# Kernel tuning notes

Measured on AMD Instinct MI355X. Metric: run time of the kernel, lower is better.

## Reference

```python
import jax, jax.numpy as jnp
import numpy as np

EPS = 1e-6

def elu_feature_map(x):
    # phi(x) = elu(x) + 1 (always positive)
    return jax.nn.elu(x) + 1.0

def setup_inputs() -> dict:
    key = jax.random.key(0)
    kq, kk, kv = jax.random.split(key, 3)
    B, T, H, E = 2, 4096, 8, 64
    return {
        "query": jax.random.normal(kq, (B, T, H, E), dtype=jnp.float32),
        "key": jax.random.normal(kk, (B, T, H, E), dtype=jnp.float32),
        "value": jax.random.normal(kv, (B, T, H, E), dtype=jnp.float32),
    }

def reference(query, key, value):
    # b t h e -> b h t e
    q = jnp.transpose(query, (0, 2, 1, 3))
    k = jnp.transpose(key, (0, 2, 1, 3))
    v = jnp.transpose(value, (0, 2, 1, 3))
    Q = elu_feature_map(q)  # [b,h,t,e]
    K = elu_feature_map(k)  # [b,h,t,e]
    # Causal linear attention: running sums over the sequence axis.
    # KV_cum[t] = sum_{s<=t} K_s (outer) V_s  -> [b,h,t,e,d]
    kv = jnp.einsum('bhte,bhtd->bhted', K, v)
    kv_cum = jnp.cumsum(kv, axis=2)
    k_cum = jnp.cumsum(K, axis=2)  # [b,h,t,e]
    # Normalizer Z_t = 1 / (Q_t . sum_{s<=t} K_s + eps)
    Z = 1.0 / (jnp.einsum('bhte,bhte->bht', Q, k_cum) + EPS)
    out = jnp.einsum('bhte,bhted->bhtd', Q, kv_cum) * Z[..., None]
    # b h t d -> b t h d
    return jnp.transpose(out, (0, 2, 1, 3))
```

## Files before the change

kernel.cpp:

```cpp
#include <hip/hip_runtime.h>
#include <hip/hip_bf16.h>
#include <math.h>

#define B 2
#define T 4096
#define H 8
#define E 64
#define D 64
#define C 128
#define NC (T / C)
#define BH (B * H)
#define EPS 1e-6f
#define PT 132
#define PQ 72
#define PBT 200

typedef short short8 __attribute__((ext_vector_type(8)));
typedef float f32x4 __attribute__((ext_vector_type(4)));

__device__ __forceinline__ float phi(float x) {
    return x > 0.0f ? x + 1.0f : __expf(x);
}
__device__ __forceinline__ uint pk2(float a, float b) {
    __hip_bfloat162 h = __float22bfloat162_rn(make_float2(a, b));
    union { __hip_bfloat162 h2; uint u; } cv; cv.h2 = h; return cv.u;
}
__device__ __forceinline__ ushort f2bf(float f) {
    uint u = __float_as_uint(f);
    return (ushort)((u + 0x7FFFu + ((u >> 16) & 1u)) >> 16);
}
__device__ __forceinline__ float bf2f(ushort h) {
    return __uint_as_float(((uint)h) << 16);
}

__global__ __launch_bounds__(256) void k_chunk_sums(
        const float* __restrict__ Kg, const float* __restrict__ Vg,
        ushort* __restrict__ SpartBf, float* __restrict__ zpart,
        ushort* __restrict__ VTg, ushort* __restrict__ PKg) {
    int blk = blockIdx.x;
    int bh = blk / NC, c = blk % NC;
    int b = bh / H, h = bh % H;
    int t0 = c * C;
    __shared__ ushort sKt[E][PT];
    __shared__ ushort sVt[D][PT];
    int tid = threadIdx.x;
    int lane = tid & 63, w = tid >> 6;
    const float4* Kg4 = (const float4*)Kg;
    const float4* Vg4 = (const float4*)Vg;
    uint2* PK2 = (uint2*)(PKg + (size_t)blk * (C * E));

    for (int l = tid; l < (C / 2) * 16; l += 256) {
        int i2 = l >> 4, e4 = l & 15;
        int t = i2 * 2;
        size_t g0 = ((size_t)(b * T + t0 + t) * H + h) * 16 + e4;
        size_t g1 = g0 + H * 16;
        float4 ka = Kg4[g0], kb = Kg4[g1];
        float4 va = Vg4[g0], vb = Vg4[g1];
        float pk0[4] = {phi(ka.x), phi(ka.y), phi(ka.z), phi(ka.w)};
        float pk1[4] = {phi(kb.x), phi(kb.y), phi(kb.z), phi(kb.w)};
        float pv0[4] = {va.x, va.y, va.z, va.w};
        float pv1[4] = {vb.x, vb.y, vb.z, vb.w};
        #pragma unroll
        for (int cc = 0; cc < 4; ++cc) {
            *(uint*)&sKt[e4 * 4 + cc][t] = pk2(pk0[cc], pk1[cc]);
            *(uint*)&sVt[e4 * 4 + cc][t] = pk2(pv0[cc], pv1[cc]);
        }
        PK2[t * 16 + e4]       = make_uint2(pk2(pk0[0], pk0[1]), pk2(pk0[2], pk0[3]));
        PK2[(t + 1) * 16 + e4] = make_uint2(pk2(pk1[0], pk1[1]), pk2(pk1[2], pk1[3]));
    }
    __syncthreads();

    {
        int g = lane >> 4, cl = lane & 15;
        int mt = w;
        f32x4 acc[4] = {};
        for (int ks = 0; ks < 4; ++ks) {
            short8 a = *(const short8*)&sKt[mt * 16 + cl][ks * 32 + g * 8];
            #pragma unroll
            for (int nt = 0; nt < 4; ++nt) {
                short8 bb = *(const short8*)&sVt[nt * 16 + cl][ks * 32 + g * 8];
                acc[nt] = __builtin_amdgcn_mfma_f32_16x16x32_bf16(a, bb, acc[nt], 0, 0, 0);
            }
        }
        ushort* Sp = SpartBf + (size_t)blk * (E * D);
        #pragma unroll
        for (int nt = 0; nt < 4; ++nt) {
            int d = nt * 16 + cl;
            *(uint2*)&Sp[d * E + mt * 16 + g * 4] =
                make_uint2(pk2(acc[nt][0], acc[nt][1]), pk2(acc[nt][2], acc[nt][3]));
        }
    }
    ushort* vt = VTg + (size_t)blk * (C * D);
    for (int l = tid; l < C * D / 8; l += 256)
        *(short8*)&vt[(l >> 4) * C + (l & 15) * 8] = *(const short8*)&sVt[l >> 4][(l & 15) * 8];
    if (tid < E) {
        float s = 0.0f;
        #pragma unroll
        for (int p = 0; p < 16; ++p) {
            short8 v = *(const short8*)&sKt[tid][p * 8];
            #pragma unroll
            for (int j = 0; j < 8; ++j) s += bf2f((ushort)v[j]);
        }
        zpart[(size_t)blk * E + tid] = s;
    }
}

__global__ __launch_bounds__(256) void k_scan(
        const ushort* __restrict__ SpartBf, float* __restrict__ zpart,
        ushort* __restrict__ S0bf) {
    int bh  = blockIdx.x / 17;
    int sub = blockIdx.x % 17;
    int tid = threadIdx.x;
    if (sub < 16) {
        int l = sub * 256 + tid;
        const ushort* base = SpartBf + (size_t)bh * NC * (E * D) + l;
        ushort* obase = S0bf + (size_t)bh * NC * (E * D) + l;
        float vals[NC];
        #pragma unroll
        for (int c = 0; c < NC; ++c) vals[c] = bf2f(base[(size_t)c * (E * D)]);
        float run = 0.0f;
        #pragma unroll
        for (int c = 0; c < NC; ++c) {
            obase[(size_t)c * (E * D)] = f2bf(run);
            run += vals[c];
        }
    } else if (tid < E) {
        float* base = zpart + (size_t)bh * NC * E + tid;
        float vals[NC];
        #pragma unroll
        for (int c = 0; c < NC; ++c) vals[c] = base[(size_t)c * E];
        float run = 0.0f;
        #pragma unroll
        for (int c = 0; c < NC; ++c) {
            base[(size_t)c * E] = run;
            run += vals[c];
        }
    }
}

__global__ __launch_bounds__(512, 4) void k_output(
        const float* __restrict__ Qg, const ushort* __restrict__ PKg,
        const ushort* __restrict__ VTg, const ushort* __restrict__ S0bf,
        const float* __restrict__ zpart, float* __restrict__ Og) {
    int blk = blockIdx.x;
    int bh = blk / NC, c = blk % NC;
    int b = bh / H, h = bh % H;
    int t0 = c * C;

    __shared__ ushort sQ[C][PQ];
    __shared__ ushort sKB[13000];
    __shared__ ushort sA[C][C];

    int tid = threadIdx.x;
    int lane = tid & 63;
    int w = tid >> 6;
    int g = lane >> 4, cl = lane & 15;

    const float4* Qg4 = (const float4*)Qg;

    for (int l = tid; l < C * 8; l += 512) {
        int i = l >> 3, e8 = l & 7;
        size_t gg = ((size_t)(b * T + t0 + i) * H + h) * 16 + e8 * 2;
        float4 qa = Qg4[gg], qb = Qg4[gg + 1];
        uint4 qv = make_uint4(pk2(phi(qa.x), phi(qa.y)), pk2(phi(qa.z), phi(qa.w)),
                              pk2(phi(qb.x), phi(qb.y)), pk2(phi(qb.z), phi(qb.w)));
        *(uint4*)&sQ[i][e8 * 8] = qv;
    }
    const short8* pk8 = (const short8*)(PKg + (size_t)blk * (C * E));
    for (int l = tid; l < C * 8; l += 512)
        *(short8*)&sKB[(l >> 3) * PQ + (l & 7) * 8] = pk8[l];
    {
        uint4 zz = make_uint4(0, 0, 0, 0);
        ushort* af = (ushort*)sA;
        #pragma unroll
        for (int it = 0; it < 4; ++it)
            *(uint4*)&af[(tid + 512 * it) * 8] = zz;
    }
    const short8* vt8 = (const short8*)(VTg + (size_t)blk * (C * D));
    short8 vt0 = vt8[tid * 2], vt1 = vt8[tid * 2 + 1];
    short8 s0reg = ((const short8*)(S0bf + (size_t)blk * (E * D)))[tid];
    float zreg = (tid < E) ? zpart[(size_t)blk * E + tid] : 0.0f;
    __syncthreads();

    for (int idx = w; idx < 36; idx += 8) {
        int tr = 0;
        while ((tr + 1) * (tr + 2) / 2 <= idx) ++tr;
        int tc = idx - tr * (tr + 1) / 2;
        f32x4 acc = {};
        #pragma unroll
        for (int ks = 0; ks < 2; ++ks) {
            short8 a  = *(const short8*)&sKB[(tc * 16 + cl) * PQ + ks * 32 + g * 8];
            short8 bq = *(const short8*)&sQ[tr * 16 + cl][ks * 32 + g * 8];
            acc = __builtin_amdgcn_mfma_f32_16x16x32_bf16(a, bq, acc, 0, 0, 0);
        }
        int iq = tr * 16 + cl;
        int j0 = tc * 16 + g * 4;
        float v0 = (j0 + 0 <= iq) ? acc[0] : 0.0f;
        float v1 = (j0 + 1 <= iq) ? acc[1] : 0.0f;
        float v2 = (j0 + 2 <= iq) ? acc[2] : 0.0f;
        float v3 = (j0 + 3 <= iq) ? acc[3] : 0.0f;
        int pb = (tc * 2 + (g >> 1)) ^ (iq & 7);
        *(uint2*)&sA[iq][pb * 8 + (g & 1) * 4] = make_uint2(pk2(v0, v1), pk2(v2, v3));
    }
    __syncthreads();

    {
        int i0 = tid * 2, i1 = tid * 2 + 1;
        *(short8*)&sKB[(i0 >> 4) * PBT + (i0 & 15) * 8] = vt0;
        *(short8*)&sKB[(i1 >> 4) * PBT + (i1 & 15) * 8] = vt1;
        *(short8*)&sKB[(tid >> 3) * PBT + 128 + (tid & 7) * 8] = s0reg;
        if (tid < E) sKB[64 * PBT + 128 + tid] = f2bf(zreg);
        else if (tid < E + 16) {
            short8 ones = {16256, 16256, 16256, 16256, 16256, 16256, 16256, 16256};
            *(short8*)&sKB[64 * PBT + (tid - E) * 8] = ones;
        }
    }
    __syncthreads();

    {
        const int permv[8] = {0, 1, 2, 3, 6, 7, 4, 5};
        int mt = permv[w];
        int m0 = mt * 16;
        int arow = m0 + cl;
        int aswz = arow & 7;
        int smax = (m0 + 15) >> 5;
        f32x4 acc[5] = {};
        for (int s = 0; s <= smax; ++s) {
            short8 a = *(const short8*)&sA[arow][(((s * 4 + g) ^ aswz)) * 8];
            #pragma unroll
            for (int nt = 0; nt < 5; ++nt) {
                short8 bb = *(const short8*)&sKB[(nt * 16 + cl) * PBT + s * 32 + g * 8];
                acc[nt] = __builtin_amdgcn_mfma_f32_16x16x32_bf16(a, bb, acc[nt], 0, 0, 0);
            }
        }
        #pragma unroll
        for (int s2 = 0; s2 < 2; ++s2) {
            short8 a = *(const short8*)&sQ[arow][s2 * 32 + g * 8];
            #pragma unroll
            for (int nt = 0; nt < 5; ++nt) {
                short8 bb = *(const short8*)&sKB[(nt * 16 + cl) * PBT + 128 + s2 * 32 + g * 8];
                acc[nt] = __builtin_amdgcn_mfma_f32_16x16x32_bf16(a, bb, acc[nt], 0, 0, 0);
            }
        }
        #pragma unroll
        for (int r = 0; r < 4; ++r) {
            float den = __shfl(acc[4][r], lane & 48);
            float zi = 1.0f / (den + EPS);
            int row = m0 + g * 4 + r;
            size_t ga = ((size_t)(b * T + t0 + row) * H + h) * 64;
            #pragma unroll
            for (int nt = 0; nt < 4; ++nt)
                Og[ga + nt * 16 + cl] = acc[nt][r] * zi;
        }
    }
}

extern "C" void kernel_launch(void* const* d_in, const int* in_sizes, int n_in,
                              void* d_out, int out_size, void* d_ws, size_t ws_size,
                              hipStream_t stream) {
    const float* q = (const float*)d_in[0];
    const float* k = (const float*)d_in[1];
    const float* v = (const float*)d_in[2];
    float* out = (float*)d_out;

    ushort* SpartBf = (ushort*)d_ws;
    float*  zpart   = (float*)(SpartBf + (size_t)BH * NC * E * D);
    ushort* VTg     = (ushort*)(zpart + (size_t)BH * NC * E);
    ushort* PKg     = VTg + (size_t)BH * NC * C * D;
    ushort* S0bf    = PKg + (size_t)BH * NC * C * E;

    k_chunk_sums<<<BH * NC, 256, 0, stream>>>(k, v, SpartBf, zpart, VTg, PKg);
    k_scan<<<BH * 17, 256, 0, stream>>>(SpartBf, zpart, S0bf);
    k_output<<<BH * NC, 512, 0, stream>>>(q, PKg, VTg, S0bf, zpart, out);
}
```

Before: 31.75 us.

## Fuse chunk-sum, scan and output kernels into one cooperative grid-synced kernel

Replaces the three-kernel pipeline (chunk sums, cross-chunk scan, per-chunk output) with a single cooperative kernel that uses two grid-wide syncs between phases. The scan phase becomes a per-thread serial prefix over chunks written in place, and Q loading plus LDS zeroing are overlapped before the second sync. The aim is to remove kernel launch gaps and inter-kernel round trips. In exchange the whole grid must be co-resident, grid-barrier overhead is added, and the old path is kept as a fallback when occupancy is too low.

```diff
diff --git a/kernel.cpp b/kernel.cpp
--- a/kernel.cpp
+++ b/kernel.cpp
@@ -1,6 +1,9 @@
 #include <hip/hip_runtime.h>
+#include <hip/hip_cooperative_groups.h>
 #include <hip/hip_bf16.h>
 #include <math.h>
+
+namespace cg = cooperative_groups;
 
 #define B 2
 #define T 4096
@@ -31,6 +34,216 @@
 }
 __device__ __forceinline__ float bf2f(ushort h) {
     return __uint_as_float(((uint)h) << 16);
+}
+
+__global__ __launch_bounds__(512, 4) void k_fused(
+        const float* __restrict__ Qg, const float* __restrict__ Kg,
+        const float* __restrict__ Vg, ushort* __restrict__ SpartBf,
+        float* __restrict__ zpart, ushort* __restrict__ VTg,
+        ushort* __restrict__ PKg, float* __restrict__ Og) {
+    __shared__ union {
+        struct { ushort Kt[E][PT]; ushort Vt[D][PT]; } p1;
+        struct { ushort Q[C][PQ]; ushort KB[13000]; ushort A[C * C]; } p3;
+    } sm;
+
+    int blk = blockIdx.x;
+    int bh = blk / NC, c = blk % NC;
+    int b = bh / H, h = bh % H;
+    int t0 = c * C;
+    int tid = threadIdx.x;
+    int lane = tid & 63, w = tid >> 6;
+    int g = lane >> 4, cl = lane & 15;
+
+    const float4* Kg4 = (const float4*)Kg;
+    const float4* Vg4 = (const float4*)Vg;
+    const float4* Qg4 = (const float4*)Qg;
+
+    {
+        uint2* PK2 = (uint2*)(PKg + (size_t)blk * (C * E));
+        for (int l = tid; l < (C / 2) * 16; l += 512) {
+            int i2 = l >> 4, e4 = l & 15;
+            int t = i2 * 2;
+            size_t g0 = ((size_t)(b * T + t0 + t) * H + h) * 16 + e4;
+            size_t g1 = g0 + H * 16;
+            float4 ka = Kg4[g0], kb = Kg4[g1];
+            float4 va = Vg4[g0], vb = Vg4[g1];
+            float pk0[4] = {phi(ka.x), phi(ka.y), phi(ka.z), phi(ka.w)};
+            float pk1[4] = {phi(kb.x), phi(kb.y), phi(kb.z), phi(kb.w)};
+            float pv0[4] = {va.x, va.y, va.z, va.w};
+            float pv1[4] = {vb.x, vb.y, vb.z, vb.w};
+            #pragma unroll
+            for (int cc = 0; cc < 4; ++cc) {
+                *(uint*)&sm.p1.Kt[e4 * 4 + cc][t] = pk2(pk0[cc], pk1[cc]);
+                *(uint*)&sm.p1.Vt[e4 * 4 + cc][t] = pk2(pv0[cc], pv1[cc]);
+            }
+            PK2[t * 16 + e4]       = make_uint2(pk2(pk0[0], pk0[1]), pk2(pk0[2], pk0[3]));
+            PK2[(t + 1) * 16 + e4] = make_uint2(pk2(pk1[0], pk1[1]), pk2(pk1[2], pk1[3]));
+        }
+        __syncthreads();
+        {
+            int mt = w >> 1;
+            f32x4 acc[2] = {};
+            for (int ks = 0; ks < 4; ++ks) {
+                short8 a = *(const short8*)&sm.p1.Kt[mt * 16 + cl][ks * 32 + g * 8];
+                #pragma unroll
+                for (int u = 0; u < 2; ++u) {
+                    int nt = (w & 1) * 2 + u;
+                    short8 bb = *(const short8*)&sm.p1.Vt[nt * 16 + cl][ks * 32 + g * 8];
+                    acc[u] = __builtin_amdgcn_mfma_f32_16x16x32_bf16(a, bb, acc[u], 0, 0, 0);
+                }
+            }
+            ushort* Sp = SpartBf + (size_t)blk * (E * D);
+            #pragma unroll
+            for (int u = 0; u < 2; ++u) {
+                int d = ((w & 1) * 2 + u) * 16 + cl;
+                *(uint2*)&Sp[d * E + mt * 16 + g * 4] =
+                    make_uint2(pk2(acc[u][0], acc[u][1]), pk2(acc[u][2], acc[u][3]));
+            }
+        }
+        ushort* vt = VTg + (size_t)blk * (C * D);
+        for (int l = tid; l < C * D / 8; l += 512)
+            *(short8*)&vt[(l >> 4) * C + (l & 15) * 8] =
+                *(const short8*)&sm.p1.Vt[l >> 4][(l & 15) * 8];
+        if (tid < E) {
+            float s = 0.0f;
+            #pragma unroll
+            for (int p = 0; p < 16; ++p) {
+                short8 v = *(const short8*)&sm.p1.Kt[tid][p * 8];
+                #pragma unroll
+                for (int j = 0; j < 8; ++j) s += bf2f((ushort)v[j]);
+            }
+            zpart[(size_t)blk * E + tid] = s;
+        }
+    }
+    __threadfence();
+    cg::this_grid().sync();
+
+    {
+        int gtid = blk * 512 + tid;
+        if (gtid < BH * E * D) {
+            int sbh = gtid >> 12, l = gtid & 4095;
+            ushort* base = SpartBf + (size_t)sbh * NC * (E * D) + l;
+            float vals[NC];
+            #pragma unroll
+            for (int c2 = 0; c2 < NC; ++c2) vals[c2] = bf2f(base[(size_t)c2 * (E * D)]);
+            float run = 0.0f;
+            #pragma unroll
+            for (int c2 = 0; c2 < NC; ++c2) {
+                base[(size_t)c2 * (E * D)] = f2bf(run);
+                run += vals[c2];
+            }
+        } else if (gtid < BH * E * D + BH * E) {
+            int idx = gtid - BH * E * D;
+            int sbh = idx >> 6, e = idx & 63;
+            float* basez = zpart + (size_t)sbh * NC * E + e;
+            float vals[NC];
+            #pragma unroll
+            for (int c2 = 0; c2 < NC; ++c2) vals[c2] = basez[(size_t)c2 * E];
+            float run = 0.0f;
+            #pragma unroll
+            for (int c2 = 0; c2 < NC; ++c2) {
+                basez[(size_t)c2 * E] = run;
+                run += vals[c2];
+            }
+        }
+    }
+    for (int l = tid; l < C * 8; l += 512) {
+        int i = l >> 3, e8 = l & 7;
+        size_t gg = ((size_t)(b * T + t0 + i) * H + h) * 16 + e8 * 2;
+        float4 qa = Qg4[gg], qb = Qg4[gg + 1];
+        uint4 qv = make_uint4(pk2(phi(qa.x), phi(qa.y)), pk2(phi(qa.z), phi(qa.w)),
+                              pk2(phi(qb.x), phi(qb.y)), pk2(phi(qb.z), phi(qb.w)));
+        *(uint4*)&sm.p3.Q[i][e8 * 8] = qv;
+    }
+    {
+        uint4 zz = make_uint4(0, 0, 0, 0);
+        #pragma unroll
+        for (int it = 0; it < 4; ++it)
+            *(uint4*)&sm.p3.A[(tid + 512 * it) * 8] = zz;
+    }
+    const short8* vt8 = (const short8*)(VTg + (size_t)blk * (C * D));
+    short8 vt0 = vt8[tid * 2], vt1 = vt8[tid * 2 + 1];
+    __threadfence();
+    cg::this_grid().sync();
+
+    short8 s0reg = ((const short8*)(SpartBf + (size_t)blk * (E * D)))[tid];
+    float zreg = (tid < E) ? zpart[(size_t)blk * E + tid] : 0.0f;
+    const short8* pk8 = (const short8*)(PKg + (size_t)blk * (C * E));
+    for (int l = tid; l < C * 8; l += 512)
+        *(short8*)&sm.p3.KB[(l >> 3) * PQ + (l & 7) * 8] = pk8[l];
+    __syncthreads();
+
+    for (int idx = w; idx < 36; idx += 8) {
+        int tr = 0;
+        while ((tr + 1) * (tr + 2) / 2 <= idx) ++tr;
+        int tc = idx - tr * (tr + 1) / 2;
+        f32x4 acc = {};
+        #pragma unroll
+        for (int ks = 0; ks < 2; ++ks) {
+            short8 a  = *(const short8*)&sm.p3.KB[(tc * 16 + cl) * PQ + ks * 32 + g * 8];
+            short8 bq = *(const short8*)&sm.p3.Q[tr * 16 + cl][ks * 32 + g * 8];
+            acc = __builtin_amdgcn_mfma_f32_16x16x32_bf16(a, bq, acc, 0, 0, 0);
+        }
+        int iq = tr * 16 + cl;
+        int j0 = tc * 16 + g * 4;
+        float v0 = (j0 + 0 <= iq) ? acc[0] : 0.0f;
+        float v1 = (j0 + 1 <= iq) ? acc[1] : 0.0f;
+        float v2 = (j0 + 2 <= iq) ? acc[2] : 0.0f;
+        float v3 = (j0 + 3 <= iq) ? acc[3] : 0.0f;
+        int pb = (tc * 2 + (g >> 1)) ^ (iq & 7);
+        *(uint2*)&sm.p3.A[iq * C + pb * 8 + (g & 1) * 4] = make_uint2(pk2(v0, v1), pk2(v2, v3));
+    }
+    __syncthreads();
+
+    {
+        int i0 = tid * 2, i1 = tid * 2 + 1;
+        *(short8*)&sm.p3.KB[(i0 >> 4) * PBT + (i0 & 15) * 8] = vt0;
+        *(short8*)&sm.p3.KB[(i1 >> 4) * PBT + (i1 & 15) * 8] = vt1;
+        *(short8*)&sm.p3.KB[(tid >> 3) * PBT + 128 + (tid & 7) * 8] = s0reg;
+        if (tid < E) sm.p3.KB[64 * PBT + 128 + tid] = f2bf(zreg);
+        else if (tid < E + 16) {
+            short8 ones = {16256, 16256, 16256, 16256, 16256, 16256, 16256, 16256};
+            *(short8*)&sm.p3.KB[64 * PBT + (tid - E) * 8] = ones;
+        }
+    }
+    __syncthreads();
+
+    {
+        const int permv[8] = {0, 1, 2, 3, 6, 7, 4, 5};
+        int mt = permv[w];
+        int m0 = mt * 16;
+        int arow = m0 + cl;
+        int aswz = arow & 7;
+        int smax = (m0 + 15) >> 5;
+        f32x4 acc[5] = {};
+        for (int s = 0; s <= smax; ++s) {
+            short8 a = *(const short8*)&sm.p3.A[arow * C + (((s * 4 + g) ^ aswz)) * 8];
+            #pragma unroll
+            for (int nt = 0; nt < 5; ++nt) {
+                short8 bb = *(const short8*)&sm.p3.KB[(nt * 16 + cl) * PBT + s * 32 + g * 8];
+                acc[nt] = __builtin_amdgcn_mfma_f32_16x16x32_bf16(a, bb, acc[nt], 0, 0, 0);
+            }
+        }
+        #pragma unroll
+        for (int s2 = 0; s2 < 2; ++s2) {
+            short8 a = *(const short8*)&sm.p3.Q[arow][s2 * 32 + g * 8];
+            #pragma unroll
+            for (int nt = 0; nt < 5; ++nt) {
+                short8 bb = *(const short8*)&sm.p3.KB[(nt * 16 + cl) * PBT + 128 + s2 * 32 + g * 8];
+                acc[nt] = __builtin_amdgcn_mfma_f32_16x16x32_bf16(a, bb, acc[nt], 0, 0, 0);
+            }
+        }
+        #pragma unroll
+        for (int r = 0; r < 4; ++r) {
+            float den = __shfl(acc[4][r], lane & 48);
+            float zi = 1.0f / (den + EPS);
+            int row = m0 + g * 4 + r;
+            size_t ga = ((size_t)(b * T + t0 + row) * H + h) * 64;
+            #pragma unroll
+            for (int nt = 0; nt < 4; ++nt)
+                Og[ga + nt * 16 + cl] = acc[nt][r] * zi;
+        }
+    }
 }
 
 __global__ __launch_bounds__(256) void k_chunk_sums(
@@ -69,7 +282,6 @@
         PK2[(t + 1) * 16 + e4] = make_uint2(pk2(pk1[0], pk1[1]), pk2(pk1[2], pk1[3]));
     }
     __syncthreads();
-
     {
         int g = lane >> 4, cl = lane & 15;
         int mt = w;
@@ -269,7 +481,15 @@
     ushort* PKg     = VTg + (size_t)BH * NC * C * D;
     ushort* S0bf    = PKg + (size_t)BH * NC * C * E;
 
-    k_chunk_sums<<<BH * NC, 256, 0, stream>>>(k, v, SpartBf, zpart, VTg, PKg);
-    k_scan<<<BH * 17, 256, 0, stream>>>(SpartBf, zpart, S0bf);
-    k_output<<<BH * NC, 512, 0, stream>>>(q, PKg, VTg, S0bf, zpart, out);
-}
+    int maxb = 0;
+    hipError_t oerr = hipOccupancyMaxActiveBlocksPerMultiprocessor(&maxb, k_fused, 512, 0);
+    if (oerr == hipSuccess && maxb >= 2) {
+        void* params[] = {(void*)&q, (void*)&k, (void*)&v, (void*)&SpartBf,
+                          (void*)&zpart, (void*)&VTg, (void*)&PKg, (void*)&out};
+        hipLaunchCooperativeKernel(k_fused, dim3(BH * NC), dim3(512), params, 0, stream);
+    } else {
+        k_chunk_sums<<<BH * NC, 256, 0, stream>>>(k, v, SpartBf, zpart, VTg, PKg);
+        k_scan<<<BH * 17, 256, 0, stream>>>(SpartBf, zpart, S0bf);
+        k_output<<<BH * NC, 512, 0, stream>>>(q, PKg, VTg, S0bf, zpart, out);
+    }
+}
```

Result: no change. 31.85 us (+0.3%).

## Transpose output MFMA, keep S0/z fragments in registers, vectorize stores

Applied to the files above, without the earlier changes.

The output kernel now loads S0 and z fragments straight from global into registers and runs the Q·S0 inter-chunk term inside the phase that builds the attention-score tile, before the barrier. That removes staging S0/z through LDS and shrinks the shared buffer. The output MFMA swaps operands so each lane holds four consecutive output columns, which allows float4 global stores instead of scalar stores and removes the shuffle for the denominator. The trade-off is more live registers for the s0f/zf fragments under launch bounds of 512 threads × 4 blocks.

```diff
diff --git a/kernel.cpp b/kernel.cpp
--- a/kernel.cpp
+++ b/kernel.cpp
@@ -13,7 +13,7 @@
 #define EPS 1e-6f
 #define PT 132
 #define PQ 72
-#define PBT 200
+#define PV 136
 
 typedef short short8 __attribute__((ext_vector_type(8)));
 typedef float f32x4 __attribute__((ext_vector_type(4)));
@@ -148,13 +148,17 @@
     int t0 = c * C;
 
     __shared__ ushort sQ[C][PQ];
-    __shared__ ushort sKB[13000];
+    __shared__ ushort sKB[9216];
     __shared__ ushort sA[C][C];
 
     int tid = threadIdx.x;
     int lane = tid & 63;
     int w = tid >> 6;
     int g = lane >> 4, cl = lane & 15;
+
+    const int permv[8] = {0, 1, 2, 3, 6, 7, 4, 5};
+    int rt = permv[w];
+    int arow = rt * 16 + cl;
 
     const float4* Qg4 = (const float4*)Qg;
 
@@ -178,79 +182,87 @@
     }
     const short8* vt8 = (const short8*)(VTg + (size_t)blk * (C * D));
     short8 vt0 = vt8[tid * 2], vt1 = vt8[tid * 2 + 1];
-    short8 s0reg = ((const short8*)(S0bf + (size_t)blk * (E * D)))[tid];
-    float zreg = (tid < E) ? zpart[(size_t)blk * E + tid] : 0.0f;
-    __syncthreads();
+    const ushort* S0p = S0bf + (size_t)blk * (E * D);
+    short8 s0f[4][2];
+    #pragma unroll
+    for (int nt = 0; nt < 4; ++nt)
+        #pragma unroll
+        for (int s2 = 0; s2 < 2; ++s2)
+            s0f[nt][s2] = *(const short8*)&S0p[(nt * 16 + cl) * E + s2 * 32 + g * 8];
+    const float* zp = zpart + (size_t)blk * E;
+    short8 zf[2];
+    #pragma unroll
+    for (int s2 = 0; s2 < 2; ++s2) {
+        int e0 = s2 * 32 + g * 8;
+        float4 za = *(const float4*)&zp[e0];
+        float4 zb = *(const float4*)&zp[e0 + 4];
+        uint4 zu = make_uint4(pk2(za.x, za.y), pk2(za.z, za.w),
+                              pk2(zb.x, zb.y), pk2(zb.z, zb.w));
+        zf[s2] = *(short8*)&zu;
+    }
+    __syncthreads();
+
+    f32x4 acc[5] = {};
 
     for (int idx = w; idx < 36; idx += 8) {
         int tr = 0;
         while ((tr + 1) * (tr + 2) / 2 <= idx) ++tr;
         int tc = idx - tr * (tr + 1) / 2;
-        f32x4 acc = {};
+        f32x4 sacc = {};
         #pragma unroll
         for (int ks = 0; ks < 2; ++ks) {
             short8 a  = *(const short8*)&sKB[(tc * 16 + cl) * PQ + ks * 32 + g * 8];
             short8 bq = *(const short8*)&sQ[tr * 16 + cl][ks * 32 + g * 8];
-            acc = __builtin_amdgcn_mfma_f32_16x16x32_bf16(a, bq, acc, 0, 0, 0);
+            sacc = __builtin_amdgcn_mfma_f32_16x16x32_bf16(a, bq, sacc, 0, 0, 0);
         }
         int iq = tr * 16 + cl;
         int j0 = tc * 16 + g * 4;
-        float v0 = (j0 + 0 <= iq) ? acc[0] : 0.0f;
-        float v1 = (j0 + 1 <= iq) ? acc[1] : 0.0f;
-        float v2 = (j0 + 2 <= iq) ? acc[2] : 0.0f;
-        float v3 = (j0 + 3 <= iq) ? acc[3] : 0.0f;
+        float v0 = (j0 + 0 <= iq) ? sacc[0] : 0.0f;
+        float v1 = (j0 + 1 <= iq) ? sacc[1] : 0.0f;
+        float v2 = (j0 + 2 <= iq) ? sacc[2] : 0.0f;
+        float v3 = (j0 + 3 <= iq) ? sacc[3] : 0.0f;
         int pb = (tc * 2 + (g >> 1)) ^ (iq & 7);
         *(uint2*)&sA[iq][pb * 8 + (g & 1) * 4] = make_uint2(pk2(v0, v1), pk2(v2, v3));
     }
+    #pragma unroll
+    for (int s2 = 0; s2 < 2; ++s2) {
+        short8 bq = *(const short8*)&sQ[arow][s2 * 32 + g * 8];
+        #pragma unroll
+        for (int nt = 0; nt < 4; ++nt)
+            acc[nt] = __builtin_amdgcn_mfma_f32_16x16x32_bf16(s0f[nt][s2], bq, acc[nt], 0, 0, 0);
+        acc[4] = __builtin_amdgcn_mfma_f32_16x16x32_bf16(zf[s2], bq, acc[4], 0, 0, 0);
+    }
     __syncthreads();
 
     {
         int i0 = tid * 2, i1 = tid * 2 + 1;
-        *(short8*)&sKB[(i0 >> 4) * PBT + (i0 & 15) * 8] = vt0;
-        *(short8*)&sKB[(i1 >> 4) * PBT + (i1 & 15) * 8] = vt1;
-        *(short8*)&sKB[(tid >> 3) * PBT + 128 + (tid & 7) * 8] = s0reg;
-        if (tid < E) sKB[64 * PBT + 128 + tid] = f2bf(zreg);
-        else if (tid < E + 16) {
-            short8 ones = {16256, 16256, 16256, 16256, 16256, 16256, 16256, 16256};
-            *(short8*)&sKB[64 * PBT + (tid - E) * 8] = ones;
-        }
-    }
-    __syncthreads();
-
-    {
-        const int permv[8] = {0, 1, 2, 3, 6, 7, 4, 5};
-        int mt = permv[w];
-        int m0 = mt * 16;
-        int arow = m0 + cl;
+        *(short8*)&sKB[(i0 >> 4) * PV + (i0 & 15) * 8] = vt0;
+        *(short8*)&sKB[(i1 >> 4) * PV + (i1 & 15) * 8] = vt1;
+    }
+    __syncthreads();
+
+    {
+        const short8 ones = {16256, 16256, 16256, 16256, 16256, 16256, 16256, 16256};
         int aswz = arow & 7;
-        int smax = (m0 + 15) >> 5;
-        f32x4 acc[5] = {};
+        int smax = (rt * 16 + 15) >> 5;
         for (int s = 0; s <= smax; ++s) {
-            short8 a = *(const short8*)&sA[arow][(((s * 4 + g) ^ aswz)) * 8];
+            short8 bs = *(const short8*)&sA[arow][(((s * 4 + g) ^ aswz)) * 8];
             #pragma unroll
-            for (int nt = 0; nt < 5; ++nt) {
-                short8 bb = *(const short8*)&sKB[(nt * 16 + cl) * PBT + s * 32 + g * 8];
-                acc[nt] = __builtin_amdgcn_mfma_f32_16x16x32_bf16(a, bb, acc[nt], 0, 0, 0);
+            for (int nt = 0; nt < 4; ++nt) {
+                short8 a = *(const short8*)&sKB[(nt * 16 + cl) * PV + s * 32 + g * 8];
+                acc[nt] = __builtin_amdgcn_mfma_f32_16x16x32_bf16(a, bs, acc[nt], 0, 0, 0);
             }
-        }
-        #pragma unroll
-        for (int s2 = 0; s2 < 2; ++s2) {
-            short8 a = *(const short8*)&sQ[arow][s2 * 32 + g * 8];
-            #pragma unroll
-            for (int nt = 0; nt < 5; ++nt) {
-                short8 bb = *(const short8*)&sKB[(nt * 16 + cl) * PBT + 128 + s2 * 32 + g * 8];
-                acc[nt] = __builtin_amdgcn_mfma_f32_16x16x32_bf16(a, bb, acc[nt], 0, 0, 0);
-            }
-        }
-        #pragma unroll
-        for (int r = 0; r < 4; ++r) {
-            float den = __shfl(acc[4][r], lane & 48);
-            float zi = 1.0f / (den + EPS);
-            int row = m0 + g * 4 + r;
-            size_t ga = ((size_t)(b * T + t0 + row) * H + h) * 64;
-            #pragma unroll
-            for (int nt = 0; nt < 4; ++nt)
-                Og[ga + nt * 16 + cl] = acc[nt][r] * zi;
+            acc[4] = __builtin_amdgcn_mfma_f32_16x16x32_bf16(ones, bs, acc[4], 0, 0, 0);
+        }
+        int row = rt * 16 + cl;
+        float den = acc[4][0];
+        float zi = 1.0f / (den + EPS);
+        size_t ga = ((size_t)(b * T + t0 + row) * H + h) * 64;
+        #pragma unroll
+        for (int nt = 0; nt < 4; ++nt) {
+            float4 o = make_float4(acc[nt][0] * zi, acc[nt][1] * zi,
+                                   acc[nt][2] * zi, acc[nt][3] * zi);
+            *(float4*)&Og[ga + nt * 16 + g * 4] = o;
         }
     }
 }
```

After: 34.02 us. +7.1%, slower.
